# Optimization experiments

Hardware: AMD Instinct MI355X
Metric: run time of the kernel (lower is better)

Reference implementation:

```python
import jax, jax.numpy as jnp
import numpy as np

NUM_HEADS = 8      # in_channels // num_head_channels = 512 // 64
NUM_GROUPS = 32    # GroupNorm groups
EPS = 1e-5


def setup_inputs() -> dict:
    key = jax.random.key(0)
    ks = jax.random.split(key, 6)
    C = 512
    x = jax.random.normal(ks[0], (8, C, 32, 32), dtype=jnp.float32)
    gn_w = jax.random.normal(ks[1], (C,), dtype=jnp.float32) * 0.1 + 1.0
    gn_b = jax.random.normal(ks[2], (C,), dtype=jnp.float32) * 0.1
    qkv_w = jax.random.normal(ks[3], (3 * C, C), dtype=jnp.float32) / np.sqrt(C)
    qkv_b = jnp.zeros((3 * C,), dtype=jnp.float32)
    # NOTE: original zero-initializes to_out; we use small random weights so the
    # attention path contributes to the output (math is identical).
    out_w = jax.random.normal(ks[4], (C, C), dtype=jnp.float32) * 0.02
    out_b = jax.random.normal(ks[5], (C,), dtype=jnp.float32) * 0.02
    return {"x": x, "gn_w": gn_w, "gn_b": gn_b, "qkv_w": qkv_w,
            "qkv_b": qkv_b, "out_w": out_w, "out_b": out_b}


def _group_norm(net, gn_w, gn_b):
    b, c, t = net.shape
    g = net.reshape(b, NUM_GROUPS, c // NUM_GROUPS, t)
    mu = jnp.mean(g, axis=(2, 3), keepdims=True)
    var = jnp.var(g, axis=(2, 3), keepdims=True)
    n = ((g - mu) * jax.lax.rsqrt(var + EPS)).reshape(b, c, t)
    return n * gn_w[None, :, None] + gn_b[None, :, None]


def reference(x, gn_w, gn_b, qkv_w, qkv_b, out_w, out_b):
    b, c, h, w = x.shape
    area = h * w
    inp = x.reshape(b, c, area)                      # [b, c, t]
    n = _group_norm(inp, gn_w, gn_b)
    # 1x1 conv1d == channel GEMM
    qkv = jnp.einsum('oc,bct->bot', qkv_w, n) + qkv_b[None, :, None]  # [b, 3c, t]
    hd = c // NUM_HEADS
    # split_qkv_after_heads: view(b*H, 3*hd, area) then split along channel
    qkv = qkv.reshape(b * NUM_HEADS, 3 * hd, area)
    q, k, v = qkv[:, :hd], qkv[:, hd:2 * hd], qkv[:, 2 * hd:]
    scale = 1.0 / np.sqrt(np.sqrt(hd))               # sqrt-sqrt per-tensor scale
    attn = jnp.einsum('bct,bcs->bts', q * scale, k * scale)  # [bH, t, s]
    prob = jax.nn.softmax(attn, axis=-1)
    net = jnp.einsum('bts,bcs->bct', prob, v).reshape(b, c, area)
    out = jnp.einsum('oc,bct->bot', out_w, net) + out_b[None, :, None]
    return (inp + out).reshape(b, c, h, w)
```

## Files before the change

kernel.cpp:

```cpp
#include <hip/hip_runtime.h>
#include <hip/hip_bf16.h>

typedef __bf16 bf16_t;
typedef __bf16 bf16x8 __attribute__((ext_vector_type(8)));
typedef __bf16 bf16x4 __attribute__((ext_vector_type(4)));
typedef float f32x4 __attribute__((ext_vector_type(4)));

#define B_DIM 8
#define C_DIM 512
#define T_DIM 1024
#define NH 8
#define HD 64

__global__ __launch_bounds__(256) void prep_w(const float* __restrict__ w1,
                                              const float* __restrict__ w2,
                                              bf16_t* __restrict__ o1,
                                              bf16_t* __restrict__ o2)
{
    int tid = blockIdx.x * 256 + threadIdx.x;
    for (int p = 0; p < 4; ++p) {
        int q = tid + p * 65536;
        const f32x4* src;
        bf16x4* dst;
        int qq;
        if (q < 196608) { src = (const f32x4*)w1; dst = (bf16x4*)o1; qq = q; }
        else            { src = (const f32x4*)w2; dst = (bf16x4*)o2; qq = q - 196608; }
        f32x4 f = src[qq];
        bf16x4 h;
        for (int j = 0; j < 4; ++j) h[j] = (bf16_t)f[j];
        dst[qq] = h;
    }
}

__global__ __launch_bounds__(256) void gn_kernel(const float* __restrict__ x,
                                                 const float* __restrict__ gw,
                                                 const float* __restrict__ gb,
                                                 bf16_t* __restrict__ n_t)
{
    __shared__ bf16_t sX[16384];
    __shared__ float sred[8];
    int tid = threadIdx.x;
    int bb  = blockIdx.x >> 5;
    int g   = blockIdx.x & 31;
    const f32x4* xg4 = reinterpret_cast<const f32x4*>(x + (size_t)(bb * C_DIM + g * 16) * T_DIM);

    float s = 0.f, sq = 0.f;
    for (int i = 0; i < 16; ++i) {
        int v = tid + i * 256;
        f32x4 f = xg4[v];
        bf16x4 h;
        for (int j = 0; j < 4; ++j) {
            s += f[j]; sq += f[j] * f[j];
            h[j] = (bf16_t)f[j];
        }
        *reinterpret_cast<bf16x4*>(sX + v * 4) = h;
    }
    for (int off = 1; off < 64; off <<= 1) {
        s  += __shfl_xor(s, off);
        sq += __shfl_xor(sq, off);
    }
    int wv = tid >> 6;
    if ((tid & 63) == 0) { sred[wv * 2] = s; sred[wv * 2 + 1] = sq; }
    __syncthreads();
    s  = sred[0] + sred[2] + sred[4] + sred[6];
    sq = sred[1] + sred[3] + sred[5] + sred[7];
    float mean = s * (1.f / 16384.f);
    float var  = sq * (1.f / 16384.f) - mean * mean;
    float rs   = rsqrtf(var + 1e-5f);

    int hf = tid & 1;
    float aa[8], bbias[8];
    for (int j = 0; j < 8; ++j) {
        int c = hf * 8 + j;
        float av = gw[g * 16 + c] * rs;
        aa[j] = av;
        bbias[j] = gb[g * 16 + c] - mean * av;
    }
    bf16_t* ob = n_t + (size_t)bb * T_DIM * C_DIM + g * 16 + hf * 8;
    for (int p = 0; p < 8; ++p) {
        int t = (tid >> 1) + p * 128;
        bf16x8 o;
        for (int j = 0; j < 8; ++j) {
            float xv = (float)sX[(hf * 8 + j) * 1024 + t];
            o[j] = (bf16_t)(xv * aa[j] + bbias[j]);
        }
        *reinterpret_cast<bf16x8*>(ob + (size_t)t * C_DIM) = o;
    }
}

__global__ __launch_bounds__(256) void qkv_gemm_kernel(
    const bf16_t* __restrict__ wqb, const float* __restrict__ bq,
    const bf16_t* __restrict__ n_t, bf16_t* __restrict__ qkv)
{
    __shared__ bf16_t sA[64 * 72];
    __shared__ bf16_t sB[128 * 72];
    int tid = threadIdx.x;
    int w = tid >> 6, lane = tid & 63, quad = lane >> 4, l15 = lane & 15;
    int bx = blockIdx.x;
    int t0 = blockIdx.y * 128;
    int bb = blockIdx.z;
    int o0 = bx * 64;
    const bf16_t* Ab = wqb + (size_t)o0 * C_DIM;
    const bf16_t* Bb = n_t + ((size_t)bb * T_DIM + t0) * C_DIM;

    f32x4 acc[2][4];
    for (int mt = 0; mt < 2; ++mt)
        for (int nt = 0; nt < 4; ++nt)
            acc[mt][nt] = f32x4{0.f, 0.f, 0.f, 0.f};
    int mw0 = (w >> 1) * 32;
    int nw0 = (w & 1) * 64;

    for (int k0 = 0; k0 < C_DIM; k0 += 64) {
        for (int i = 0; i < 2; ++i) {
            int v = tid + i * 256;
            int row = v >> 3, c8 = v & 7;
            *reinterpret_cast<bf16x8*>(sA + row * 72 + c8 * 8) =
                *reinterpret_cast<const bf16x8*>(Ab + (size_t)row * C_DIM + k0 + c8 * 8);
        }
        for (int i = 0; i < 4; ++i) {
            int v = tid + i * 256;
            int row = v >> 3, c8 = v & 7;
            *reinterpret_cast<bf16x8*>(sB + row * 72 + c8 * 8) =
                *reinterpret_cast<const bf16x8*>(Bb + (size_t)row * C_DIM + k0 + c8 * 8);
        }
        __syncthreads();
        for (int kk = 0; kk < 2; ++kk) {
            bf16x8 af[2], bfr[4];
            for (int mt = 0; mt < 2; ++mt)
                af[mt] = *reinterpret_cast<const bf16x8*>(sA + (mw0 + mt * 16 + l15) * 72 + kk * 32 + quad * 8);
            for (int nt = 0; nt < 4; ++nt)
                bfr[nt] = *reinterpret_cast<const bf16x8*>(sB + (nw0 + nt * 16 + l15) * 72 + kk * 32 + quad * 8);
            for (int mt = 0; mt < 2; ++mt)
                for (int nt = 0; nt < 4; ++nt)
                    acc[mt][nt] = __builtin_amdgcn_mfma_f32_16x16x32_bf16(af[mt], bfr[nt], acc[mt][nt], 0, 0, 0);
        }
        __syncthreads();
    }

    int h = bx / 3, type = bx % 3;
    size_t base = ((size_t)(bb * NH + h) * 3 + type) * (64 * 1024);

    if (type < 2) {
        for (int mt = 0; mt < 2; ++mt)
            for (int nt = 0; nt < 4; ++nt)
                for (int r = 0; r < 4; ++r) {
                    int mw = mw0 + mt * 16 + quad * 4 + r;
                    int tl = nw0 + nt * 16 + l15;
                    float v = acc[mt][nt][r] + bq[o0 + mw];
                    sB[tl * 72 + mw] = (bf16_t)v;
                }
        __syncthreads();
        for (int i = 0; i < 4; ++i) {
            int v = tid + i * 256;
            int tl = v >> 3, c8 = v & 7;
            bf16x8 d = *reinterpret_cast<const bf16x8*>(sB + tl * 72 + c8 * 8);
            *reinterpret_cast<bf16x8*>(qkv + base + (size_t)(t0 + tl) * 64 + c8 * 8) = d;
        }
    } else {
        for (int mt = 0; mt < 2; ++mt)
            for (int nt = 0; nt < 4; ++nt)
                for (int r = 0; r < 4; ++r) {
                    int mw = mw0 + mt * 16 + quad * 4 + r;
                    int tl = nw0 + nt * 16 + l15;
                    float v = acc[mt][nt][r] + bq[o0 + mw];
                    sB[mw * 136 + tl] = (bf16_t)v;
                }
        __syncthreads();
        for (int i = 0; i < 4; ++i) {
            int v = tid + i * 256;
            int cc = v >> 4, t8 = (v & 15) * 8;
            bf16x8 d = *reinterpret_cast<const bf16x8*>(sB + cc * 136 + t8);
            *reinterpret_cast<bf16x8*>(qkv + base + (size_t)cc * 1024 + t0 + t8) = d;
        }
    }
}

__global__ __launch_bounds__(256, 4) void attn_kernel(const bf16_t* __restrict__ qkv,
                                                      bf16_t* __restrict__ net_t)
{
    __shared__ bf16_t sQ[64 * 72];
    __shared__ bf16_t sK[64 * 72];
    __shared__ bf16_t sV[64 * 72];
    __shared__ bf16_t sP[4][16 * 72];
    int tid = threadIdx.x;
    int w = tid >> 6, lane = tid & 63, quad = lane >> 4, l15 = lane & 15;
    int bh = blockIdx.x;
    int qt = blockIdx.y;
    size_t qb = (size_t)bh * 3 * 65536;
    const bf16_t* Qg = qkv + qb + (size_t)qt * 4096;
    const bf16_t* Kg = qkv + qb + 65536;
    const bf16_t* Vg = qkv + qb + 2 * 65536;

    for (int i = 0; i < 2; ++i) {
        int v = tid + i * 256;
        *reinterpret_cast<bf16x8*>(sQ + (v >> 3) * 72 + (v & 7) * 8) =
            *reinterpret_cast<const bf16x8*>(Qg + v * 8);
    }

    bf16x8 kreg[2], vreg[2];
    for (int i = 0; i < 2; ++i) {
        int v = tid + i * 256;
        kreg[i] = *reinterpret_cast<const bf16x8*>(Kg + (size_t)(v >> 3) * 64 + (v & 7) * 8);
        vreg[i] = *reinterpret_cast<const bf16x8*>(Vg + (size_t)(v >> 3) * 1024 + (v & 7) * 8);
    }

    f32x4 O[4];
    for (int i = 0; i < 4; ++i) O[i] = f32x4{0.f, 0.f, 0.f, 0.f};
    float lsum[4] = {0.f, 0.f, 0.f, 0.f};
    const float K2 = 0.125f * 1.44269504088896f;
    bf16_t* sPw = sP[w];

    for (int st = 0; st < 16; ++st) {
        __syncthreads();
        for (int i = 0; i < 2; ++i) {
            int v = tid + i * 256;
            *reinterpret_cast<bf16x8*>(sK + (v >> 3) * 72 + (v & 7) * 8) = kreg[i];
            *reinterpret_cast<bf16x8*>(sV + (v >> 3) * 72 + (v & 7) * 8) = vreg[i];
        }
        __syncthreads();
        if (st < 15) {
            int s0 = (st + 1) * 64;
            for (int i = 0; i < 2; ++i) {
                int v = tid + i * 256;
                kreg[i] = *reinterpret_cast<const bf16x8*>(Kg + (size_t)(s0 + (v >> 3)) * 64 + (v & 7) * 8);
                vreg[i] = *reinterpret_cast<const bf16x8*>(Vg + (size_t)(v >> 3) * 1024 + s0 + (v & 7) * 8);
            }
        }

        f32x4 Sacc[4];
        for (int nt = 0; nt < 4; ++nt) Sacc[nt] = f32x4{0.f, 0.f, 0.f, 0.f};
        for (int kk = 0; kk < 2; ++kk) {
            bf16x8 af = *reinterpret_cast<const bf16x8*>(sQ + (w * 16 + l15) * 72 + kk * 32 + quad * 8);
            for (int nt = 0; nt < 4; ++nt) {
                bf16x8 bfr = *reinterpret_cast<const bf16x8*>(sK + (nt * 16 + l15) * 72 + kk * 32 + quad * 8);
                Sacc[nt] = __builtin_amdgcn_mfma_f32_16x16x32_bf16(af, bfr, Sacc[nt], 0, 0, 0);
            }
        }

        for (int nt = 0; nt < 4; ++nt)
            for (int r = 0; r < 4; ++r) {
                float p = exp2f(Sacc[nt][r] * K2);
                lsum[r] += p;
                sPw[(quad * 4 + r) * 72 + nt * 16 + l15] = (bf16_t)p;
            }

        for (int ks = 0; ks < 2; ++ks) {
            bf16x8 af = *reinterpret_cast<const bf16x8*>(sPw + l15 * 72 + ks * 32 + quad * 8);
            for (int nt2 = 0; nt2 < 4; ++nt2) {
                bf16x8 bfr = *reinterpret_cast<const bf16x8*>(sV + (nt2 * 16 + l15) * 72 + ks * 32 + quad * 8);
                O[nt2] = __builtin_amdgcn_mfma_f32_16x16x32_bf16(af, bfr, O[nt2], 0, 0, 0);
            }
        }
    }

    float inv[4];
    for (int r = 0; r < 4; ++r) {
        float l = lsum[r];
        for (int off = 1; off < 16; off <<= 1) l += __shfl_xor(l, off);
        inv[r] = 1.f / l;
    }
    int bb = bh >> 3, h = bh & 7;
    for (int nt2 = 0; nt2 < 4; ++nt2)
        for (int r = 0; r < 4; ++r) {
            int t = qt * 64 + w * 16 + quad * 4 + r;
            int c = h * 64 + nt2 * 16 + l15;
            net_t[((size_t)bb * T_DIM + t) * C_DIM + c] = (bf16_t)(O[nt2][r] * inv[r]);
        }
}

__global__ __launch_bounds__(256) void out_gemm_kernel(
    const bf16_t* __restrict__ wob, const float* __restrict__ bo,
    const bf16_t* __restrict__ net_t, const float* __restrict__ x,
    float* __restrict__ out)
{
    __shared__ bf16_t sA[64 * 72];
    __shared__ bf16_t sB[128 * 72];
    int tid = threadIdx.x;
    int w = tid >> 6, lane = tid & 63, quad = lane >> 4, l15 = lane & 15;
    int o0 = blockIdx.x * 64;
    int t0 = blockIdx.y * 128;
    int bb = blockIdx.z;
    const bf16_t* Ab = wob + (size_t)o0 * C_DIM;
    const bf16_t* Bb = net_t + ((size_t)bb * T_DIM + t0) * C_DIM;

    f32x4 acc[2][4];
    for (int mt = 0; mt < 2; ++mt)
        for (int nt = 0; nt < 4; ++nt)
            acc[mt][nt] = f32x4{0.f, 0.f, 0.f, 0.f};
    int mw0 = (w >> 1) * 32;
    int nw0 = (w & 1) * 64;

    for (int k0 = 0; k0 < C_DIM; k0 += 64) {
        for (int i = 0; i < 2; ++i) {
            int v = tid + i * 256;
            int row = v >> 3, c8 = v & 7;
            *reinterpret_cast<bf16x8*>(sA + row * 72 + c8 * 8) =
                *reinterpret_cast<const bf16x8*>(Ab + (size_t)row * C_DIM + k0 + c8 * 8);
        }
        for (int i = 0; i < 4; ++i) {
            int v = tid + i * 256;
            int row = v >> 3, c8 = v & 7;
            *reinterpret_cast<bf16x8*>(sB + row * 72 + c8 * 8) =
                *reinterpret_cast<const bf16x8*>(Bb + (size_t)row * C_DIM + k0 + c8 * 8);
        }
        __syncthreads();
        for (int kk = 0; kk < 2; ++kk) {
            bf16x8 af[2], bfr[4];
            for (int mt = 0; mt < 2; ++mt)
                af[mt] = *reinterpret_cast<const bf16x8*>(sA + (mw0 + mt * 16 + l15) * 72 + kk * 32 + quad * 8);
            for (int nt = 0; nt < 4; ++nt)
                bfr[nt] = *reinterpret_cast<const bf16x8*>(sB + (nw0 + nt * 16 + l15) * 72 + kk * 32 + quad * 8);
            for (int mt = 0; mt < 2; ++mt)
                for (int nt = 0; nt < 4; ++nt)
                    acc[mt][nt] = __builtin_amdgcn_mfma_f32_16x16x32_bf16(af[mt], bfr[nt], acc[mt][nt], 0, 0, 0);
        }
        __syncthreads();
    }

    for (int mt = 0; mt < 2; ++mt)
        for (int nt = 0; nt < 4; ++nt)
            for (int r = 0; r < 4; ++r) {
                int o = o0 + mw0 + mt * 16 + quad * 4 + r;
                int t = t0 + nw0 + nt * 16 + l15;
                size_t idx = ((size_t)bb * C_DIM + o) * T_DIM + t;
                out[idx] = acc[mt][nt][r] + bo[o] + x[idx];
            }
}

extern "C" void kernel_launch(void* const* d_in, const int* in_sizes, int n_in,
                              void* d_out, int out_size, void* d_ws, size_t ws_size,
                              hipStream_t stream)
{
    const float* x     = (const float*)d_in[0];
    const float* gn_w  = (const float*)d_in[1];
    const float* gn_b  = (const float*)d_in[2];
    const float* qkv_w = (const float*)d_in[3];
    const float* qkv_b = (const float*)d_in[4];
    const float* out_w = (const float*)d_in[5];
    const float* out_b = (const float*)d_in[6];
    float* out = (float*)d_out;

    char* ws = (char*)d_ws;
    bf16_t* n_t   = (bf16_t*)(ws);
    bf16_t* qkv   = (bf16_t*)(ws + 8388608);
    bf16_t* net_t = (bf16_t*)(ws + 33554432);
    bf16_t* wqb   = (bf16_t*)(ws + 41943040);
    bf16_t* wob   = (bf16_t*)(ws + 41943040 + 1572864);

    prep_w<<<dim3(256), 256, 0, stream>>>(qkv_w, out_w, wqb, wob);
    gn_kernel<<<dim3(256), 256, 0, stream>>>(x, gn_w, gn_b, n_t);
    qkv_gemm_kernel<<<dim3(24, 8, 8), 256, 0, stream>>>(wqb, qkv_b, n_t, qkv);
    attn_kernel<<<dim3(64, 16), 256, 0, stream>>>(qkv, net_t);
    out_gemm_kernel<<<dim3(8, 8, 8), 256, 0, stream>>>(wob, out_b, net_t, x, out);
}
```

Before: 165.9 us.

## Load attention Q/K/V fragments directly from global memory instead of LDS

The attention kernel no longer stages Q, K and V tiles in shared memory with block-wide barriers. Each wave loads its MFMA operand fragments straight from global memory, relying on L1/L2 caching, and drops the per-tile __syncthreads. The PV product is transposed (V as the A operand, P as B) so the output fragment can be written as contiguous bf16x4 stores, and row sums are exchanged through a small LDS array. This trades LDS staging and barrier stalls for more, less coalesced global loads, with no explicit prefetch overlap.

```diff
diff --git a/kernel.cpp b/kernel.cpp
--- a/kernel.cpp
+++ b/kernel.cpp
@@ -178,10 +178,8 @@
 __global__ __launch_bounds__(256, 4) void attn_kernel(const bf16_t* __restrict__ qkv,
                                                       bf16_t* __restrict__ net_t)
 {
-    __shared__ bf16_t sQ[64 * 72];
-    __shared__ bf16_t sK[64 * 72];
-    __shared__ bf16_t sV[64 * 72];
     __shared__ bf16_t sP[4][16 * 72];
+    __shared__ float  sL[4][16];
     int tid = threadIdx.x;
     int w = tid >> 6, lane = tid & 63, quad = lane >> 4, l15 = lane & 15;
     int bh = blockIdx.x;
@@ -190,52 +188,28 @@
     const bf16_t* Qg = qkv + qb + (size_t)qt * 4096;
     const bf16_t* Kg = qkv + qb + 65536;
     const bf16_t* Vg = qkv + qb + 2 * 65536;
-
-    for (int i = 0; i < 2; ++i) {
-        int v = tid + i * 256;
-        *reinterpret_cast<bf16x8*>(sQ + (v >> 3) * 72 + (v & 7) * 8) =
-            *reinterpret_cast<const bf16x8*>(Qg + v * 8);
-    }
-
-    bf16x8 kreg[2], vreg[2];
-    for (int i = 0; i < 2; ++i) {
-        int v = tid + i * 256;
-        kreg[i] = *reinterpret_cast<const bf16x8*>(Kg + (size_t)(v >> 3) * 64 + (v & 7) * 8);
-        vreg[i] = *reinterpret_cast<const bf16x8*>(Vg + (size_t)(v >> 3) * 1024 + (v & 7) * 8);
-    }
+    const float K2 = 0.125f * 1.44269504088896f;
+
+    bf16x8 qf[2];
+    for (int kk = 0; kk < 2; ++kk)
+        qf[kk] = *reinterpret_cast<const bf16x8*>(Qg + (size_t)(w * 16 + l15) * 64 + kk * 32 + quad * 8);
 
     f32x4 O[4];
     for (int i = 0; i < 4; ++i) O[i] = f32x4{0.f, 0.f, 0.f, 0.f};
     float lsum[4] = {0.f, 0.f, 0.f, 0.f};
-    const float K2 = 0.125f * 1.44269504088896f;
     bf16_t* sPw = sP[w];
 
     for (int st = 0; st < 16; ++st) {
-        __syncthreads();
-        for (int i = 0; i < 2; ++i) {
-            int v = tid + i * 256;
-            *reinterpret_cast<bf16x8*>(sK + (v >> 3) * 72 + (v & 7) * 8) = kreg[i];
-            *reinterpret_cast<bf16x8*>(sV + (v >> 3) * 72 + (v & 7) * 8) = vreg[i];
-        }
-        __syncthreads();
-        if (st < 15) {
-            int s0 = (st + 1) * 64;
-            for (int i = 0; i < 2; ++i) {
-                int v = tid + i * 256;
-                kreg[i] = *reinterpret_cast<const bf16x8*>(Kg + (size_t)(s0 + (v >> 3)) * 64 + (v & 7) * 8);
-                vreg[i] = *reinterpret_cast<const bf16x8*>(Vg + (size_t)(v >> 3) * 1024 + s0 + (v & 7) * 8);
-            }
-        }
+        int s0 = st * 64;
 
         f32x4 Sacc[4];
         for (int nt = 0; nt < 4; ++nt) Sacc[nt] = f32x4{0.f, 0.f, 0.f, 0.f};
-        for (int kk = 0; kk < 2; ++kk) {
-            bf16x8 af = *reinterpret_cast<const bf16x8*>(sQ + (w * 16 + l15) * 72 + kk * 32 + quad * 8);
+        for (int kk = 0; kk < 2; ++kk)
             for (int nt = 0; nt < 4; ++nt) {
-                bf16x8 bfr = *reinterpret_cast<const bf16x8*>(sK + (nt * 16 + l15) * 72 + kk * 32 + quad * 8);
-                Sacc[nt] = __builtin_amdgcn_mfma_f32_16x16x32_bf16(af, bfr, Sacc[nt], 0, 0, 0);
+                bf16x8 kf = *reinterpret_cast<const bf16x8*>(
+                    Kg + (size_t)(s0 + nt * 16 + l15) * 64 + kk * 32 + quad * 8);
+                Sacc[nt] = __builtin_amdgcn_mfma_f32_16x16x32_bf16(qf[kk], kf, Sacc[nt], 0, 0, 0);
             }
-        }
 
         for (int nt = 0; nt < 4; ++nt)
             for (int r = 0; r < 4; ++r) {
@@ -244,28 +218,32 @@
                 sPw[(quad * 4 + r) * 72 + nt * 16 + l15] = (bf16_t)p;
             }
 
-        for (int ks = 0; ks < 2; ++ks) {
-            bf16x8 af = *reinterpret_cast<const bf16x8*>(sPw + l15 * 72 + ks * 32 + quad * 8);
-            for (int nt2 = 0; nt2 < 4; ++nt2) {
-                bf16x8 bfr = *reinterpret_cast<const bf16x8*>(sV + (nt2 * 16 + l15) * 72 + ks * 32 + quad * 8);
-                O[nt2] = __builtin_amdgcn_mfma_f32_16x16x32_bf16(af, bfr, O[nt2], 0, 0, 0);
+        bf16x8 pf[2];
+        for (int ks = 0; ks < 2; ++ks)
+            pf[ks] = *reinterpret_cast<const bf16x8*>(sPw + l15 * 72 + ks * 32 + quad * 8);
+        for (int ks = 0; ks < 2; ++ks)
+            for (int mt = 0; mt < 4; ++mt) {
+                bf16x8 vf = *reinterpret_cast<const bf16x8*>(
+                    Vg + (size_t)(mt * 16 + l15) * 1024 + s0 + ks * 32 + quad * 8);
+                O[mt] = __builtin_amdgcn_mfma_f32_16x16x32_bf16(vf, pf[ks], O[mt], 0, 0, 0);
             }
-        }
-    }
-
-    float inv[4];
+    }
+
     for (int r = 0; r < 4; ++r) {
         float l = lsum[r];
         for (int off = 1; off < 16; off <<= 1) l += __shfl_xor(l, off);
-        inv[r] = 1.f / l;
-    }
+        if (l15 == 0) sL[w][quad * 4 + r] = l;
+    }
+    float inv = 1.f / sL[w][l15];
+
     int bb = bh >> 3, h = bh & 7;
-    for (int nt2 = 0; nt2 < 4; ++nt2)
-        for (int r = 0; r < 4; ++r) {
-            int t = qt * 64 + w * 16 + quad * 4 + r;
-            int c = h * 64 + nt2 * 16 + l15;
-            net_t[((size_t)bb * T_DIM + t) * C_DIM + c] = (bf16_t)(O[nt2][r] * inv[r]);
-        }
+    int t = qt * 64 + w * 16 + l15;
+    bf16_t* orow = net_t + ((size_t)bb * T_DIM + t) * C_DIM + h * 64;
+    for (int mt = 0; mt < 4; ++mt) {
+        bf16x4 o4;
+        for (int r = 0; r < 4; ++r) o4[r] = (bf16_t)(O[mt][r] * inv);
+        *reinterpret_cast<bf16x4*>(orow + mt * 16 + quad * 4) = o4;
+    }
 }
 
 __global__ __launch_bounds__(256) void out_gemm_kernel(
```

Result: slower. 240.2 us (+44.7%).

## Keep attention P in registers via transposed S=K·Qᵀ and 16x16x16 MFMA for PV

Applied to the files above, without the earlier changes.

Reworks the attention inner loop so S is computed transposed (K as the A operand, Q fragments held in registers), which leaves each lane holding a column of probabilities. That layout feeds the PV product directly through the 16x16x16 bf16 MFMA with no shared-memory round trip for P. The sQ and sP shared buffers are removed, the occupancy hint rises from 4 to 6 blocks, the row-sum reduction shrinks to two shuffles, and outputs are written as 4-wide vector stores. The cost is more, smaller MFMA instructions and more register pressure under the tighter launch bound.

```diff
diff --git a/kernel.cpp b/kernel.cpp
--- a/kernel.cpp
+++ b/kernel.cpp
@@ -4,13 +4,19 @@
 typedef __bf16 bf16_t;
 typedef __bf16 bf16x8 __attribute__((ext_vector_type(8)));
 typedef __bf16 bf16x4 __attribute__((ext_vector_type(4)));
-typedef float f32x4 __attribute__((ext_vector_type(4)));
+typedef short  s16x4  __attribute__((ext_vector_type(4)));
+typedef float  f32x4  __attribute__((ext_vector_type(4)));
 
 #define B_DIM 8
 #define C_DIM 512
 #define T_DIM 1024
 #define NH 8
 #define HD 64
+
+__device__ __forceinline__ f32x4 mfma16_bf16(bf16x4 a, bf16x4 b, f32x4 c) {
+    return __builtin_amdgcn_mfma_f32_16x16x16bf16_1k(
+        __builtin_bit_cast(s16x4, a), __builtin_bit_cast(s16x4, b), c, 0, 0, 0);
+}
 
 __global__ __launch_bounds__(256) void prep_w(const float* __restrict__ w1,
                                               const float* __restrict__ w2,
@@ -175,13 +181,11 @@
     }
 }
 
-__global__ __launch_bounds__(256, 4) void attn_kernel(const bf16_t* __restrict__ qkv,
+__global__ __launch_bounds__(256, 6) void attn_kernel(const bf16_t* __restrict__ qkv,
                                                       bf16_t* __restrict__ net_t)
 {
-    __shared__ bf16_t sQ[64 * 72];
     __shared__ bf16_t sK[64 * 72];
     __shared__ bf16_t sV[64 * 72];
-    __shared__ bf16_t sP[4][16 * 72];
     int tid = threadIdx.x;
     int w = tid >> 6, lane = tid & 63, quad = lane >> 4, l15 = lane & 15;
     int bh = blockIdx.x;
@@ -190,12 +194,11 @@
     const bf16_t* Qg = qkv + qb + (size_t)qt * 4096;
     const bf16_t* Kg = qkv + qb + 65536;
     const bf16_t* Vg = qkv + qb + 2 * 65536;
-
-    for (int i = 0; i < 2; ++i) {
-        int v = tid + i * 256;
-        *reinterpret_cast<bf16x8*>(sQ + (v >> 3) * 72 + (v & 7) * 8) =
-            *reinterpret_cast<const bf16x8*>(Qg + v * 8);
-    }
+    const float K2 = 0.125f * 1.44269504088896f;
+
+    bf16x8 qf[2];
+    for (int kk = 0; kk < 2; ++kk)
+        qf[kk] = *reinterpret_cast<const bf16x8*>(Qg + (size_t)(w * 16 + l15) * 64 + kk * 32 + quad * 8);
 
     bf16x8 kreg[2], vreg[2];
     for (int i = 0; i < 2; ++i) {
@@ -206,9 +209,7 @@
 
     f32x4 O[4];
     for (int i = 0; i < 4; ++i) O[i] = f32x4{0.f, 0.f, 0.f, 0.f};
-    float lsum[4] = {0.f, 0.f, 0.f, 0.f};
-    const float K2 = 0.125f * 1.44269504088896f;
-    bf16_t* sPw = sP[w];
+    float lsum = 0.f;
 
     for (int st = 0; st < 16; ++st) {
         __syncthreads();
@@ -219,53 +220,45 @@
         }
         __syncthreads();
         if (st < 15) {
-            int s0 = (st + 1) * 64;
+            int s0n = (st + 1) * 64;
             for (int i = 0; i < 2; ++i) {
                 int v = tid + i * 256;
-                kreg[i] = *reinterpret_cast<const bf16x8*>(Kg + (size_t)(s0 + (v >> 3)) * 64 + (v & 7) * 8);
-                vreg[i] = *reinterpret_cast<const bf16x8*>(Vg + (size_t)(v >> 3) * 1024 + s0 + (v & 7) * 8);
-            }
-        }
-
-        f32x4 Sacc[4];
-        for (int nt = 0; nt < 4; ++nt) Sacc[nt] = f32x4{0.f, 0.f, 0.f, 0.f};
-        for (int kk = 0; kk < 2; ++kk) {
-            bf16x8 af = *reinterpret_cast<const bf16x8*>(sQ + (w * 16 + l15) * 72 + kk * 32 + quad * 8);
-            for (int nt = 0; nt < 4; ++nt) {
-                bf16x8 bfr = *reinterpret_cast<const bf16x8*>(sK + (nt * 16 + l15) * 72 + kk * 32 + quad * 8);
-                Sacc[nt] = __builtin_amdgcn_mfma_f32_16x16x32_bf16(af, bfr, Sacc[nt], 0, 0, 0);
-            }
-        }
-
-        for (int nt = 0; nt < 4; ++nt)
+                kreg[i] = *reinterpret_cast<const bf16x8*>(Kg + (size_t)(s0n + (v >> 3)) * 64 + (v & 7) * 8);
+                vreg[i] = *reinterpret_cast<const bf16x8*>(Vg + (size_t)(v >> 3) * 1024 + s0n + (v & 7) * 8);
+            }
+        }
+
+        for (int mt = 0; mt < 4; ++mt) {
+            f32x4 S = f32x4{0.f, 0.f, 0.f, 0.f};
+            for (int kk = 0; kk < 2; ++kk) {
+                bf16x8 kf = *reinterpret_cast<const bf16x8*>(sK + (mt * 16 + l15) * 72 + kk * 32 + quad * 8);
+                S = __builtin_amdgcn_mfma_f32_16x16x32_bf16(kf, qf[kk], S, 0, 0, 0);
+            }
+            bf16x4 pf;
             for (int r = 0; r < 4; ++r) {
-                float p = exp2f(Sacc[nt][r] * K2);
-                lsum[r] += p;
-                sPw[(quad * 4 + r) * 72 + nt * 16 + l15] = (bf16_t)p;
-            }
-
-        for (int ks = 0; ks < 2; ++ks) {
-            bf16x8 af = *reinterpret_cast<const bf16x8*>(sPw + l15 * 72 + ks * 32 + quad * 8);
-            for (int nt2 = 0; nt2 < 4; ++nt2) {
-                bf16x8 bfr = *reinterpret_cast<const bf16x8*>(sV + (nt2 * 16 + l15) * 72 + ks * 32 + quad * 8);
-                O[nt2] = __builtin_amdgcn_mfma_f32_16x16x32_bf16(af, bfr, O[nt2], 0, 0, 0);
-            }
-        }
-    }
-
-    float inv[4];
-    for (int r = 0; r < 4; ++r) {
-        float l = lsum[r];
-        for (int off = 1; off < 16; off <<= 1) l += __shfl_xor(l, off);
-        inv[r] = 1.f / l;
-    }
+                float p = exp2f(S[r] * K2);
+                lsum += p;
+                pf[r] = (bf16_t)p;
+            }
+            for (int ct = 0; ct < 4; ++ct) {
+                bf16x4 vf = *reinterpret_cast<const bf16x4*>(sV + (ct * 16 + l15) * 72 + mt * 16 + quad * 4);
+                O[ct] = mfma16_bf16(vf, pf, O[ct]);
+            }
+        }
+    }
+
+    lsum += __shfl_xor(lsum, 16);
+    lsum += __shfl_xor(lsum, 32);
+    float inv = 1.f / lsum;
+
     int bb = bh >> 3, h = bh & 7;
-    for (int nt2 = 0; nt2 < 4; ++nt2)
-        for (int r = 0; r < 4; ++r) {
-            int t = qt * 64 + w * 16 + quad * 4 + r;
-            int c = h * 64 + nt2 * 16 + l15;
-            net_t[((size_t)bb * T_DIM + t) * C_DIM + c] = (bf16_t)(O[nt2][r] * inv[r]);
-        }
+    int t = qt * 64 + w * 16 + l15;
+    bf16_t* orow = net_t + ((size_t)bb * T_DIM + t) * C_DIM + h * 64;
+    for (int ct = 0; ct < 4; ++ct) {
+        bf16x4 o4;
+        for (int r = 0; r < 4; ++r) o4[r] = (bf16_t)(O[ct][r] * inv);
+        *reinterpret_cast<bf16x4*>(orow + ct * 16 + quad * 4) = o4;
+    }
 }
 
 __global__ __launch_bounds__(256) void out_gemm_kernel(
```

After: 162.5 us. 1.02x faster.
